# Kernel optimization log

Measured on AMD Instinct MI355X. Metric: run time of the kernel, lower is better.

The kernel has to match this reference:

```python
import jax, jax.numpy as jnp
import numpy as np

B, T, D, H = 2, 2048, 1024, 16
DK = D // H

def setup_inputs() -> dict:
    key = jax.random.key(0)
    ks = jax.random.split(key, 12)
    s = 1.0 / np.sqrt(D)
    inp = {
        'Q': jax.random.normal(ks[0], (B, T, D), jnp.float32),
        'K': jax.random.normal(ks[1], (B, T, D), jnp.float32),
        'V': jax.random.normal(ks[2], (B, T, D), jnp.float32),
        'mask': jnp.tril(jnp.ones((T, T), jnp.int32))[None, None],  # causal [1,1,T,T]
        'Wq_w': jax.random.normal(ks[3], (D, D), jnp.float32) * s,
        'Wq_b': jax.random.normal(ks[4], (D,), jnp.float32) * s,
        'Wk_w': jax.random.normal(ks[5], (D, D), jnp.float32) * s,
        'Wk_b': jax.random.normal(ks[6], (D,), jnp.float32) * s,
        'Wv_w': jax.random.normal(ks[7], (D, D), jnp.float32) * s,
        'Wv_b': jax.random.normal(ks[8], (D,), jnp.float32) * s,
        'Wo_w': jax.random.normal(ks[9], (D, D), jnp.float32) * s,
        'Wo_b': jax.random.normal(ks[10], (D,), jnp.float32) * s,
    }
    return inp

def reference(Q, K, V, mask, Wq_w, Wq_b, Wk_w, Wk_b, Wv_w, Wv_b, Wo_w, Wo_b):
    b, tq, c = Q.shape
    tk = K.shape[1]
    q = (Q @ Wq_w + Wq_b).reshape(b, tq, H, DK).transpose(0, 2, 1, 3)  # [B,H,Tq,dk]
    k = (K @ Wk_w + Wk_b).reshape(b, tk, H, DK).transpose(0, 2, 1, 3)
    v = (V @ Wv_w + Wv_b).reshape(b, tk, H, DK).transpose(0, 2, 1, 3)
    scores = jnp.einsum('bhqd,bhkd->bhqk', q, k) / jnp.sqrt(jnp.float32(DK))
    scores = jnp.where(mask == 0, jnp.float32(-1e9), scores)
    attn = jax.nn.softmax(scores, axis=-1)
    out = jnp.einsum('bhqk,bhkd->bhqd', attn, v)
    out = out.transpose(0, 2, 1, 3).reshape(b, tq, c)
    return out @ Wo_w + Wo_b
```

## Files before the change

kernel.cpp:

```cpp
#include <hip/hip_runtime.h>
#include <hip/hip_bf16.h>

#define NB 2
#define NT 2048
#define ND 1024
#define NH 16
#define NDK 64

typedef __attribute__((ext_vector_type(8))) short bf16x8;
typedef __attribute__((ext_vector_type(4))) float f32x4;

static __device__ __forceinline__ short f2bf(float f) {
  union { float f; unsigned u; } c; c.f = f;
  unsigned u = c.u;
  u += 0x7FFF + ((u >> 16) & 1);
  return (short)(u >> 16);
}

static __device__ __forceinline__ unsigned cvt_pk_bf16(float lo, float hi) {
  unsigned r;
  asm("v_cvt_pk_bf16_f32 %0, %1, %2" : "=v"(r) : "v"(lo), "v"(hi));
  return r;
}

static __device__ __forceinline__ void gload16(const void* g, void* l) {
  __builtin_amdgcn_global_load_lds((const __attribute__((address_space(1))) void*)g,
                                   (__attribute__((address_space(3))) void*)l, 16, 0, 0);
}

__global__ void cast3_kernel(const float* __restrict__ s0, const float* __restrict__ s1,
                             const float* __restrict__ s2,
                             short* __restrict__ t0, short* __restrict__ t1,
                             short* __restrict__ t2) {
  int z = blockIdx.x >> 11;
  int i = (blockIdx.x & 2047) * 256 + threadIdx.x;
  const float* src = z == 0 ? s0 : (z == 1 ? s1 : s2);
  short* dst       = z == 0 ? t0 : (z == 1 ? t1 : t2);
  const float4* s4 = (const float4*)src + (size_t)i * 2;
  float4 a = s4[0], b = s4[1];
  bf16x8 o;
  o[0] = f2bf(a.x); o[1] = f2bf(a.y); o[2] = f2bf(a.z); o[3] = f2bf(a.w);
  o[4] = f2bf(b.x); o[5] = f2bf(b.y); o[6] = f2bf(b.z); o[7] = f2bf(b.w);
  *((bf16x8*)dst + i) = o;
}

__global__ void wtrans_kernel(const float* __restrict__ W0, const float* __restrict__ W1,
                              const float* __restrict__ W2, const float* __restrict__ W3,
                              short* __restrict__ T0, short* __restrict__ T1,
                              short* __restrict__ T2, short* __restrict__ T3) {
  __shared__ float t[32][33];
  int z = blockIdx.z;
  const float* W = z == 0 ? W0 : (z == 1 ? W1 : (z == 2 ? W2 : W3));
  short* Wt      = z == 0 ? T0 : (z == 1 ? T1 : (z == 2 ? T2 : T3));
  int n0 = blockIdx.x * 32, k0 = blockIdx.y * 32;
  int tx = threadIdx.x, ty = threadIdx.y;
  for (int i = ty; i < 32; i += 8) t[i][tx] = W[(size_t)(k0 + i) * ND + n0 + tx];
  __syncthreads();
  for (int i = ty; i < 32; i += 8) Wt[(size_t)(n0 + i) * ND + k0 + tx] = f2bf(t[tx][i]);
}

template <int MODE>
__global__ __launch_bounds__(256, 2) void gemm_bt(
    const short* __restrict__ A0, const short* __restrict__ A1, const short* __restrict__ A2,
    const short* __restrict__ W0, const short* __restrict__ W1, const short* __restrict__ W2,
    const float* __restrict__ b0, const float* __restrict__ b1, const float* __restrict__ b2,
    void* o0, void* o1, void* o2)
{
  constexpr int K = ND;
  __shared__ short As[2][128 * 32];
  __shared__ short Bs[2][128 * 32];
  int z = blockIdx.z;
  const short* A    = z == 0 ? A0 : (z == 1 ? A1 : A2);
  const short* Wt   = z == 0 ? W0 : (z == 1 ? W1 : W2);
  const float* bias = z == 0 ? b0 : (z == 1 ? b1 : b2);
  void* out         = z == 0 ? o0 : (z == 1 ? o1 : o2);
  float scl = (MODE == 0 && z == 0) ? 0.18033688011112042f : 1.0f;

  int m0 = blockIdx.y * 128, n0 = blockIdx.x * 128;
  int tid = threadIdx.x, wid = tid >> 6, lane = tid & 63;
  int wr = wid >> 1, wc = wid & 1;
  int r16 = lane & 15, l4 = lane >> 4;

  auto stage = [&](int buf, int kt) {
    int rbase = wid * 32;
    int row = rbase + (lane >> 2);
    int c8 = (lane & 3) * 8;
    const short* ga = A  + (size_t)(m0 + row) * K + kt * 32 + c8;
    const short* gb = Wt + (size_t)(n0 + row) * K + kt * 32 + c8;
    gload16(ga,          &As[buf][rbase * 32]);
    gload16(ga + 16 * K, &As[buf][(rbase + 16) * 32]);
    gload16(gb,          &Bs[buf][rbase * 32]);
    gload16(gb + 16 * K, &Bs[buf][(rbase + 16) * 32]);
  };

  f32x4 acc[4][4] = {};
  stage(0, 0);
  __syncthreads();

  for (int kt = 0; kt < K / 32; ++kt) {
    int cur = kt & 1;
    if (kt + 1 < K / 32) stage(cur ^ 1, kt + 1);
    bf16x8 af[4], bfv[4];
    int kk = l4 * 8;
#pragma unroll
    for (int mi = 0; mi < 4; mi++)
      af[mi] = *(const bf16x8*)&As[cur][(wr * 64 + mi * 16 + r16) * 32 + kk];
#pragma unroll
    for (int ni = 0; ni < 4; ni++)
      bfv[ni] = *(const bf16x8*)&Bs[cur][(wc * 64 + ni * 16 + r16) * 32 + kk];
#pragma unroll
    for (int mi = 0; mi < 4; mi++)
#pragma unroll
      for (int ni = 0; ni < 4; ni++)
        acc[mi][ni] = __builtin_amdgcn_mfma_f32_16x16x32_bf16(af[mi], bfv[ni], acc[mi][ni], 0, 0, 0);
    __syncthreads();
  }

  int mb = m0 + wr * 64, nb = n0 + wc * 64;
#pragma unroll
  for (int mi = 0; mi < 4; mi++)
#pragma unroll
    for (int ni = 0; ni < 4; ni++) {
      int n = nb + ni * 16 + r16;
      float bv = bias[n];
      if constexpr (MODE == 0) {
        int h = n >> 6, dk = n & 63;
        if (z == 2) {
          int m0_ = mb + mi * 16 + l4 * 4;
          int bI = m0_ >> 11, t0 = m0_ & (NT - 1);
          int bh = bI * NH + h;
          short4 s4;
          s4.x = f2bf(acc[mi][ni][0] + bv);
          s4.y = f2bf(acc[mi][ni][1] + bv);
          s4.z = f2bf(acc[mi][ni][2] + bv);
          s4.w = f2bf(acc[mi][ni][3] + bv);
          *(short4*)&((short*)out)[(size_t)bh * 131072 + (dk >> 4) * 32768 +
                                   (t0 >> 3) * 128 + (dk & 15) * 8 + (t0 & 7)] = s4;
        } else if (z == 1) {
#pragma unroll
          for (int r = 0; r < 4; r++) {
            int m = mb + mi * 16 + l4 * 4 + r;
            int bI = m >> 11, t = m & (NT - 1);
            int bh = bI * NH + h;
            ((short*)out)[(size_t)bh * 131072 + (t >> 4) * 1024 + (dk >> 3) * 128 +
                          (t & 15) * 8 + (dk & 7)] = f2bf(acc[mi][ni][r] + bv);
          }
        } else {
#pragma unroll
          for (int r = 0; r < 4; r++) {
            int m = mb + mi * 16 + l4 * 4 + r;
            int bI = m >> 11, t = m & (NT - 1);
            ((short*)out)[((((size_t)bI * NH + h) * NT + t) << 6) + dk] = f2bf((acc[mi][ni][r] + bv) * scl);
          }
        }
      } else {
#pragma unroll
        for (int r = 0; r < 4; r++) {
          int m = mb + mi * 16 + l4 * 4 + r;
          ((float*)out)[(size_t)m * ND + n] = acc[mi][ni][r] + bv;
        }
      }
    }
}

__global__ __launch_bounds__(256) void attn_kernel(
    const short* __restrict__ q, const short* __restrict__ k, const short* __restrict__ vt,
    short* __restrict__ O)
{
  struct SH {
    union {
      short p2[4][2][16][72];
      struct {
        f32x4 obuf[4][2][4][64];
        float ol[4][32];
      } mg;
    };
  };
  __shared__ SH sh;

  int d = blockIdx.x;
  int xcd = d & 7, jj = d >> 3;
  int bh = xcd * 4 + (jj >> 5);
  int pair = jj & 31;
  int b = bh >> 4, h = bh & 15;
  int tid = threadIdx.x, wid = tid >> 6, lane = tid & 63;
  int r16 = lane & 15, l4 = lane >> 4;
  size_t hb = (size_t)bh * NT * NDK;
  const short* qh = q + hb;
  const short* kh = k + hb;
  const short* vh = vt + hb;

#pragma unroll 1
  for (int half = 0; half < 2; ++half) {
    int qg = half == 0 ? (63 - pair) : pair;
    int qw = qg * 32;

    bf16x8 qa[2][2];
#pragma unroll
    for (int rf = 0; rf < 2; rf++)
#pragma unroll
      for (int kf = 0; kf < 2; kf++)
        qa[rf][kf] = *(const bf16x8*)(qh + (size_t)(qw + rf * 16 + r16) * NDK + kf * 32 + l4 * 8);

    f32x4 of[2][4] = {};
    float l_[2] = { 0.f, 0.f };

    int nt = (qw + 95) >> 6;
    for (int kt = wid; kt < nt; kt += 4) {
      int kv0 = kt * 64;

      f32x4 sf[2][4] = {};
      __builtin_amdgcn_s_setprio(1);
#pragma unroll
      for (int cf = 0; cf < 4; cf++) {
        const short* kb_ = kh + (size_t)((kv0 >> 4) + cf) * 1024 + lane * 8;
        bf16x8 k0 = *(const bf16x8*)kb_;
        bf16x8 k1 = *(const bf16x8*)(kb_ + 512);
        sf[0][cf] = __builtin_amdgcn_mfma_f32_16x16x32_bf16(k0, qa[0][0], sf[0][cf], 0, 0, 0);
        sf[1][cf] = __builtin_amdgcn_mfma_f32_16x16x32_bf16(k0, qa[1][0], sf[1][cf], 0, 0, 0);
        sf[0][cf] = __builtin_amdgcn_mfma_f32_16x16x32_bf16(k1, qa[0][1], sf[0][cf], 0, 0, 0);
        sf[1][cf] = __builtin_amdgcn_mfma_f32_16x16x32_bf16(k1, qa[1][1], sf[1][cf], 0, 0, 0);
      }
      __builtin_amdgcn_s_setprio(0);

      bf16x8 vb[4][2];
#pragma unroll
      for (int df = 0; df < 4; df++)
#pragma unroll
        for (int kf = 0; kf < 2; kf++)
          vb[df][kf] = *(const bf16x8*)(vh + df * 32768 + (kv0 >> 3) * 128 + kf * 512 + lane * 8);

      if (kv0 + 63 > qw) {
#pragma unroll
        for (int rf = 0; rf < 2; rf++)
#pragma unroll
          for (int cf = 0; cf < 4; cf++)
#pragma unroll
            for (int r = 0; r < 4; r++) {
              int kvi = kv0 + cf * 16 + l4 * 4 + r;
              int qi = qw + rf * 16 + r16;
              if (kvi > qi) sf[rf][cf][r] = -1e30f;
            }
      }

#pragma unroll
      for (int rf = 0; rf < 2; rf++) {
        float rs = 0.f;
#pragma unroll
        for (int cf = 0; cf < 4; cf++) {
          float p0 = __builtin_amdgcn_exp2f(sf[rf][cf][0]);
          float p1 = __builtin_amdgcn_exp2f(sf[rf][cf][1]);
          float p2v = __builtin_amdgcn_exp2f(sf[rf][cf][2]);
          float p3 = __builtin_amdgcn_exp2f(sf[rf][cf][3]);
          rs += (p0 + p1) + (p2v + p3);
          unsigned w0 = cvt_pk_bf16(p0, p1);
          unsigned w1 = cvt_pk_bf16(p2v, p3);
          *(int2*)&sh.p2[wid][rf][r16][cf * 16 + l4 * 4] = make_int2((int)w0, (int)w1);
        }
        l_[rf] += rs;
      }

      __builtin_amdgcn_s_setprio(1);
#pragma unroll
      for (int rf = 0; rf < 2; rf++)
#pragma unroll
        for (int kf = 0; kf < 2; kf++) {
          bf16x8 pa = *(const bf16x8*)&sh.p2[wid][rf][r16][kf * 32 + l4 * 8];
#pragma unroll
          for (int df = 0; df < 4; df++)
            of[rf][df] = __builtin_amdgcn_mfma_f32_16x16x32_bf16(vb[df][kf], pa, of[rf][df], 0, 0, 0);
        }
      __builtin_amdgcn_s_setprio(0);
    }

#pragma unroll
    for (int rf = 0; rf < 2; rf++) {
      float t = l_[rf];
      t += __shfl_xor(t, 16);
      t += __shfl_xor(t, 32);
      l_[rf] = t;
    }

    __syncthreads();
#pragma unroll
    for (int rf = 0; rf < 2; rf++) {
      if (l4 == 0) sh.mg.ol[wid][rf * 16 + r16] = l_[rf];
#pragma unroll
      for (int df = 0; df < 4; df++)
        sh.mg.obuf[wid][rf][df][lane] = of[rf][df];
    }
    __syncthreads();

#pragma unroll
    for (int rf = 0; rf < 2; rf++) {
      int row = rf * 16 + r16;
      float lst = sh.mg.ol[0][row] + sh.mg.ol[1][row] + sh.mg.ol[2][row] + sh.mg.ol[3][row];
      float rinv = 1.0f / lst;
      f32x4 o0 = sh.mg.obuf[0][rf][wid][lane];
      f32x4 o1 = sh.mg.obuf[1][rf][wid][lane];
      f32x4 o2 = sh.mg.obuf[2][rf][wid][lane];
      f32x4 o3 = sh.mg.obuf[3][rf][wid][lane];
      float v0 = (o0[0] + o1[0] + o2[0] + o3[0]) * rinv;
      float v1 = (o0[1] + o1[1] + o2[1] + o3[1]) * rinv;
      float v2 = (o0[2] + o1[2] + o2[2] + o3[2]) * rinv;
      float v3 = (o0[3] + o1[3] + o2[3] + o3[3]) * rinv;
      int t = qw + rf * 16 + r16;
      *(int2*)&O[(size_t)(b * NT + t) * ND + h * 64 + wid * 16 + l4 * 4] =
          make_int2((int)cvt_pk_bf16(v0, v1), (int)cvt_pk_bf16(v2, v3));
    }
    __syncthreads();
  }
}

extern "C" void kernel_launch(void* const* d_in, const int* in_sizes, int n_in,
                              void* d_out, int out_size, void* d_ws, size_t ws_size,
                              hipStream_t stream)
{
  const float* Q  = (const float*)d_in[0];
  const float* Ki = (const float*)d_in[1];
  const float* V  = (const float*)d_in[2];
  const float* Wq = (const float*)d_in[4];  const float* bq = (const float*)d_in[5];
  const float* Wk = (const float*)d_in[6];  const float* bk = (const float*)d_in[7];
  const float* Wv = (const float*)d_in[8];  const float* bv = (const float*)d_in[9];
  const float* Wo = (const float*)d_in[10]; const float* bo = (const float*)d_in[11];

  short* ws = (short*)d_ws;
  const size_t M4 = (size_t)4 * 1024 * 1024;
  short* Qb  = ws;
  short* Kb  = ws + M4;
  short* Vb  = ws + 2 * M4;
  short* qp  = ws + 3 * M4;
  short* kp  = ws + 4 * M4;
  short* vtp = ws + 5 * M4;
  short* Wqt = ws + 6 * M4;
  short* Wkt = Wqt + 1024 * 1024;
  short* Wvt = Wkt + 1024 * 1024;
  short* Wot = Wvt + 1024 * 1024;
  short* Obuf = Qb;

  cast3_kernel<<<6144, 256, 0, stream>>>(Q, Ki, V, Qb, Kb, Vb);
  wtrans_kernel<<<dim3(32, 32, 4), dim3(32, 8), 0, stream>>>(Wq, Wk, Wv, Wo,
                                                             Wqt, Wkt, Wvt, Wot);

  gemm_bt<0><<<dim3(8, 32, 3), 256, 0, stream>>>(Qb, Kb, Vb, Wqt, Wkt, Wvt,
                                                 bq, bk, bv, qp, kp, vtp);
  attn_kernel<<<1024, 256, 0, stream>>>(qp, kp, vtp, Obuf);
  gemm_bt<1><<<dim3(8, 32, 1), 256, 0, stream>>>(Obuf, Obuf, Obuf, Wot, Wot, Wot,
                                                 bo, bo, bo, d_out, d_out, d_out);
}
```

Before: 130.3 us.

## Fuse fp32-to-bf16 input cast into projection GEMM and split attention blocks per query tile

Drops the separate cast kernel. The QKV projection GEMM now loads fp32 activations directly, converts them to bf16 in registers and writes them to LDS, which removes one full write and read of the bf16 copies. The attention kernel no longer pairs a long and a short query tile per block. It launches one block per 32-row query tile, so twice as many blocks, and the merge step is done in two passes to halve the LDS buffer. In exchange, the GEMM A-loads become synchronous register loads instead of async global-to-LDS loads, and without the pairing the causal work per block is unbalanced.

```diff
diff --git a/kernel.cpp b/kernel.cpp
--- a/kernel.cpp
+++ b/kernel.cpp
@@ -26,22 +26,6 @@
 static __device__ __forceinline__ void gload16(const void* g, void* l) {
   __builtin_amdgcn_global_load_lds((const __attribute__((address_space(1))) void*)g,
                                    (__attribute__((address_space(3))) void*)l, 16, 0, 0);
-}
-
-__global__ void cast3_kernel(const float* __restrict__ s0, const float* __restrict__ s1,
-                             const float* __restrict__ s2,
-                             short* __restrict__ t0, short* __restrict__ t1,
-                             short* __restrict__ t2) {
-  int z = blockIdx.x >> 11;
-  int i = (blockIdx.x & 2047) * 256 + threadIdx.x;
-  const float* src = z == 0 ? s0 : (z == 1 ? s1 : s2);
-  short* dst       = z == 0 ? t0 : (z == 1 ? t1 : t2);
-  const float4* s4 = (const float4*)src + (size_t)i * 2;
-  float4 a = s4[0], b = s4[1];
-  bf16x8 o;
-  o[0] = f2bf(a.x); o[1] = f2bf(a.y); o[2] = f2bf(a.z); o[3] = f2bf(a.w);
-  o[4] = f2bf(b.x); o[5] = f2bf(b.y); o[6] = f2bf(b.z); o[7] = f2bf(b.w);
-  *((bf16x8*)dst + i) = o;
 }
 
 __global__ void wtrans_kernel(const float* __restrict__ W0, const float* __restrict__ W1,
@@ -61,7 +45,7 @@
 
 template <int MODE>
 __global__ __launch_bounds__(256, 2) void gemm_bt(
-    const short* __restrict__ A0, const short* __restrict__ A1, const short* __restrict__ A2,
+    const void* A0v, const void* A1v, const void* A2v,
     const short* __restrict__ W0, const short* __restrict__ W1, const short* __restrict__ W2,
     const float* __restrict__ b0, const float* __restrict__ b1, const float* __restrict__ b2,
     void* o0, void* o1, void* o2)
@@ -70,10 +54,12 @@
   __shared__ short As[2][128 * 32];
   __shared__ short Bs[2][128 * 32];
   int z = blockIdx.z;
-  const short* A    = z == 0 ? A0 : (z == 1 ? A1 : A2);
+  const void* Av    = z == 0 ? A0v : (z == 1 ? A1v : A2v);
   const short* Wt   = z == 0 ? W0 : (z == 1 ? W1 : W2);
   const float* bias = z == 0 ? b0 : (z == 1 ? b1 : b2);
   void* out         = z == 0 ? o0 : (z == 1 ? o1 : o2);
+  const float* Af = (const float*)Av;
+  const short* Ab = (const short*)Av;
   float scl = (MODE == 0 && z == 0) ? 0.18033688011112042f : 1.0f;
 
   int m0 = blockIdx.y * 128, n0 = blockIdx.x * 128;
@@ -85,10 +71,24 @@
     int rbase = wid * 32;
     int row = rbase + (lane >> 2);
     int c8 = (lane & 3) * 8;
-    const short* ga = A  + (size_t)(m0 + row) * K + kt * 32 + c8;
+    if constexpr (MODE == 0) {
+      const float* ga = Af + (size_t)(m0 + row) * K + kt * 32 + c8;
+      float4 a0 = *(const float4*)ga;
+      float4 a1 = *(const float4*)(ga + 4);
+      float4 a2 = *(const float4*)(ga + (size_t)16 * K);
+      float4 a3 = *(const float4*)(ga + (size_t)16 * K + 4);
+      int4 w0 = make_int4((int)cvt_pk_bf16(a0.x, a0.y), (int)cvt_pk_bf16(a0.z, a0.w),
+                          (int)cvt_pk_bf16(a1.x, a1.y), (int)cvt_pk_bf16(a1.z, a1.w));
+      int4 w1 = make_int4((int)cvt_pk_bf16(a2.x, a2.y), (int)cvt_pk_bf16(a2.z, a2.w),
+                          (int)cvt_pk_bf16(a3.x, a3.y), (int)cvt_pk_bf16(a3.z, a3.w));
+      *(int4*)&As[buf][row * 32 + c8] = w0;
+      *(int4*)&As[buf][(row + 16) * 32 + c8] = w1;
+    } else {
+      const short* ga = Ab + (size_t)(m0 + row) * K + kt * 32 + c8;
+      gload16(ga,          &As[buf][rbase * 32]);
+      gload16(ga + 16 * K, &As[buf][(rbase + 16) * 32]);
+    }
     const short* gb = Wt + (size_t)(n0 + row) * K + kt * 32 + c8;
-    gload16(ga,          &As[buf][rbase * 32]);
-    gload16(ga + 16 * K, &As[buf][(rbase + 16) * 32]);
     gload16(gb,          &Bs[buf][rbase * 32]);
     gload16(gb + 16 * K, &Bs[buf][(rbase + 16) * 32]);
   };
@@ -171,7 +171,7 @@
     union {
       short p2[4][2][16][72];
       struct {
-        f32x4 obuf[4][2][4][64];
+        f32x4 obuf[4][2][2][64];
         float ol[4][32];
       } mg;
     };
@@ -180,8 +180,8 @@
 
   int d = blockIdx.x;
   int xcd = d & 7, jj = d >> 3;
-  int bh = xcd * 4 + (jj >> 5);
-  int pair = jj & 31;
+  int bh = xcd * 4 + (jj >> 6);
+  int qg = 63 - (jj & 63);
   int b = bh >> 4, h = bh & 15;
   int tid = threadIdx.x, wid = tid >> 6, lane = tid & 63;
   int r16 = lane & 15, l4 = lane >> 4;
@@ -189,123 +189,122 @@
   const short* qh = q + hb;
   const short* kh = k + hb;
   const short* vh = vt + hb;
-
-#pragma unroll 1
-  for (int half = 0; half < 2; ++half) {
-    int qg = half == 0 ? (63 - pair) : pair;
-    int qw = qg * 32;
-
-    bf16x8 qa[2][2];
+  int qw = qg * 32;
+
+  bf16x8 qa[2][2];
+#pragma unroll
+  for (int rf = 0; rf < 2; rf++)
+#pragma unroll
+    for (int kf = 0; kf < 2; kf++)
+      qa[rf][kf] = *(const bf16x8*)(qh + (size_t)(qw + rf * 16 + r16) * NDK + kf * 32 + l4 * 8);
+
+  f32x4 of[2][4] = {};
+  float l_[2] = { 0.f, 0.f };
+
+  int nt = (qw + 95) >> 6;
+  for (int kt = wid; kt < nt; kt += 4) {
+    int kv0 = kt * 64;
+
+    f32x4 sf[2][4] = {};
+    __builtin_amdgcn_s_setprio(1);
+#pragma unroll
+    for (int cf = 0; cf < 4; cf++) {
+      const short* kb_ = kh + (size_t)((kv0 >> 4) + cf) * 1024 + lane * 8;
+      bf16x8 k0 = *(const bf16x8*)kb_;
+      bf16x8 k1 = *(const bf16x8*)(kb_ + 512);
+      sf[0][cf] = __builtin_amdgcn_mfma_f32_16x16x32_bf16(k0, qa[0][0], sf[0][cf], 0, 0, 0);
+      sf[1][cf] = __builtin_amdgcn_mfma_f32_16x16x32_bf16(k0, qa[1][0], sf[1][cf], 0, 0, 0);
+      sf[0][cf] = __builtin_amdgcn_mfma_f32_16x16x32_bf16(k1, qa[0][1], sf[0][cf], 0, 0, 0);
+      sf[1][cf] = __builtin_amdgcn_mfma_f32_16x16x32_bf16(k1, qa[1][1], sf[1][cf], 0, 0, 0);
+    }
+    __builtin_amdgcn_s_setprio(0);
+
+    bf16x8 vb[4][2];
+#pragma unroll
+    for (int df = 0; df < 4; df++)
+#pragma unroll
+      for (int kf = 0; kf < 2; kf++)
+        vb[df][kf] = *(const bf16x8*)(vh + df * 32768 + (kv0 >> 3) * 128 + kf * 512 + lane * 8);
+
+    if (kv0 + 63 > qw) {
+#pragma unroll
+      for (int rf = 0; rf < 2; rf++)
+#pragma unroll
+        for (int cf = 0; cf < 4; cf++)
+#pragma unroll
+          for (int r = 0; r < 4; r++) {
+            int kvi = kv0 + cf * 16 + l4 * 4 + r;
+            int qi = qw + rf * 16 + r16;
+            if (kvi > qi) sf[rf][cf][r] = -1e30f;
+          }
+    }
+
+#pragma unroll
+    for (int rf = 0; rf < 2; rf++) {
+      float rs = 0.f;
+#pragma unroll
+      for (int cf = 0; cf < 4; cf++) {
+        float p0 = __builtin_amdgcn_exp2f(sf[rf][cf][0]);
+        float p1 = __builtin_amdgcn_exp2f(sf[rf][cf][1]);
+        float p2v = __builtin_amdgcn_exp2f(sf[rf][cf][2]);
+        float p3 = __builtin_amdgcn_exp2f(sf[rf][cf][3]);
+        rs += (p0 + p1) + (p2v + p3);
+        unsigned w0 = cvt_pk_bf16(p0, p1);
+        unsigned w1 = cvt_pk_bf16(p2v, p3);
+        *(int2*)&sh.p2[wid][rf][r16][cf * 16 + l4 * 4] = make_int2((int)w0, (int)w1);
+      }
+      l_[rf] += rs;
+    }
+
+    __builtin_amdgcn_s_setprio(1);
 #pragma unroll
     for (int rf = 0; rf < 2; rf++)
 #pragma unroll
-      for (int kf = 0; kf < 2; kf++)
-        qa[rf][kf] = *(const bf16x8*)(qh + (size_t)(qw + rf * 16 + r16) * NDK + kf * 32 + l4 * 8);
-
-    f32x4 of[2][4] = {};
-    float l_[2] = { 0.f, 0.f };
-
-    int nt = (qw + 95) >> 6;
-    for (int kt = wid; kt < nt; kt += 4) {
-      int kv0 = kt * 64;
-
-      f32x4 sf[2][4] = {};
-      __builtin_amdgcn_s_setprio(1);
-#pragma unroll
-      for (int cf = 0; cf < 4; cf++) {
-        const short* kb_ = kh + (size_t)((kv0 >> 4) + cf) * 1024 + lane * 8;
-        bf16x8 k0 = *(const bf16x8*)kb_;
-        bf16x8 k1 = *(const bf16x8*)(kb_ + 512);
-        sf[0][cf] = __builtin_amdgcn_mfma_f32_16x16x32_bf16(k0, qa[0][0], sf[0][cf], 0, 0, 0);
-        sf[1][cf] = __builtin_amdgcn_mfma_f32_16x16x32_bf16(k0, qa[1][0], sf[1][cf], 0, 0, 0);
-        sf[0][cf] = __builtin_amdgcn_mfma_f32_16x16x32_bf16(k1, qa[0][1], sf[0][cf], 0, 0, 0);
-        sf[1][cf] = __builtin_amdgcn_mfma_f32_16x16x32_bf16(k1, qa[1][1], sf[1][cf], 0, 0, 0);
+      for (int kf = 0; kf < 2; kf++) {
+        bf16x8 pa = *(const bf16x8*)&sh.p2[wid][rf][r16][kf * 32 + l4 * 8];
+#pragma unroll
+        for (int df = 0; df < 4; df++)
+          of[rf][df] = __builtin_amdgcn_mfma_f32_16x16x32_bf16(vb[df][kf], pa, of[rf][df], 0, 0, 0);
       }
-      __builtin_amdgcn_s_setprio(0);
-
-      bf16x8 vb[4][2];
-#pragma unroll
-      for (int df = 0; df < 4; df++)
-#pragma unroll
-        for (int kf = 0; kf < 2; kf++)
-          vb[df][kf] = *(const bf16x8*)(vh + df * 32768 + (kv0 >> 3) * 128 + kf * 512 + lane * 8);
-
-      if (kv0 + 63 > qw) {
-#pragma unroll
-        for (int rf = 0; rf < 2; rf++)
-#pragma unroll
-          for (int cf = 0; cf < 4; cf++)
-#pragma unroll
-            for (int r = 0; r < 4; r++) {
-              int kvi = kv0 + cf * 16 + l4 * 4 + r;
-              int qi = qw + rf * 16 + r16;
-              if (kvi > qi) sf[rf][cf][r] = -1e30f;
-            }
-      }
-
-#pragma unroll
-      for (int rf = 0; rf < 2; rf++) {
-        float rs = 0.f;
-#pragma unroll
-        for (int cf = 0; cf < 4; cf++) {
-          float p0 = __builtin_amdgcn_exp2f(sf[rf][cf][0]);
-          float p1 = __builtin_amdgcn_exp2f(sf[rf][cf][1]);
-          float p2v = __builtin_amdgcn_exp2f(sf[rf][cf][2]);
-          float p3 = __builtin_amdgcn_exp2f(sf[rf][cf][3]);
-          rs += (p0 + p1) + (p2v + p3);
-          unsigned w0 = cvt_pk_bf16(p0, p1);
-          unsigned w1 = cvt_pk_bf16(p2v, p3);
-          *(int2*)&sh.p2[wid][rf][r16][cf * 16 + l4 * 4] = make_int2((int)w0, (int)w1);
-        }
-        l_[rf] += rs;
-      }
-
-      __builtin_amdgcn_s_setprio(1);
-#pragma unroll
-      for (int rf = 0; rf < 2; rf++)
-#pragma unroll
-        for (int kf = 0; kf < 2; kf++) {
-          bf16x8 pa = *(const bf16x8*)&sh.p2[wid][rf][r16][kf * 32 + l4 * 8];
-#pragma unroll
-          for (int df = 0; df < 4; df++)
-            of[rf][df] = __builtin_amdgcn_mfma_f32_16x16x32_bf16(vb[df][kf], pa, of[rf][df], 0, 0, 0);
-        }
-      __builtin_amdgcn_s_setprio(0);
-    }
-
-#pragma unroll
-    for (int rf = 0; rf < 2; rf++) {
-      float t = l_[rf];
-      t += __shfl_xor(t, 16);
-      t += __shfl_xor(t, 32);
-      l_[rf] = t;
-    }
-
+    __builtin_amdgcn_s_setprio(0);
+  }
+
+#pragma unroll
+  for (int rf = 0; rf < 2; rf++) {
+    float t = l_[rf];
+    t += __shfl_xor(t, 16);
+    t += __shfl_xor(t, 32);
+    l_[rf] = t;
+  }
+
+  __syncthreads();
+  if (l4 == 0) {
+    sh.mg.ol[wid][r16] = l_[0];
+    sh.mg.ol[wid][16 + r16] = l_[1];
+  }
+#pragma unroll
+  for (int pass = 0; pass < 2; ++pass) {
+#pragma unroll
+    for (int rf = 0; rf < 2; rf++)
+#pragma unroll
+      for (int dfp = 0; dfp < 2; dfp++)
+        sh.mg.obuf[wid][rf][dfp][lane] = of[rf][2 * pass + dfp];
     __syncthreads();
-#pragma unroll
-    for (int rf = 0; rf < 2; rf++) {
-      if (l4 == 0) sh.mg.ol[wid][rf * 16 + r16] = l_[rf];
-#pragma unroll
-      for (int df = 0; df < 4; df++)
-        sh.mg.obuf[wid][rf][df][lane] = of[rf][df];
-    }
-    __syncthreads();
-
-#pragma unroll
-    for (int rf = 0; rf < 2; rf++) {
-      int row = rf * 16 + r16;
+    {
+      int mrf = wid >> 1, mdfp = wid & 1, mdf = 2 * pass + mdfp;
+      int row = mrf * 16 + r16;
       float lst = sh.mg.ol[0][row] + sh.mg.ol[1][row] + sh.mg.ol[2][row] + sh.mg.ol[3][row];
       float rinv = 1.0f / lst;
-      f32x4 o0 = sh.mg.obuf[0][rf][wid][lane];
-      f32x4 o1 = sh.mg.obuf[1][rf][wid][lane];
-      f32x4 o2 = sh.mg.obuf[2][rf][wid][lane];
-      f32x4 o3 = sh.mg.obuf[3][rf][wid][lane];
+      f32x4 o0 = sh.mg.obuf[0][mrf][mdfp][lane];
+      f32x4 o1 = sh.mg.obuf[1][mrf][mdfp][lane];
+      f32x4 o2 = sh.mg.obuf[2][mrf][mdfp][lane];
+      f32x4 o3 = sh.mg.obuf[3][mrf][mdfp][lane];
       float v0 = (o0[0] + o1[0] + o2[0] + o3[0]) * rinv;
       float v1 = (o0[1] + o1[1] + o2[1] + o3[1]) * rinv;
       float v2 = (o0[2] + o1[2] + o2[2] + o3[2]) * rinv;
       float v3 = (o0[3] + o1[3] + o2[3] + o3[3]) * rinv;
-      int t = qw + rf * 16 + r16;
-      *(int2*)&O[(size_t)(b * NT + t) * ND + h * 64 + wid * 16 + l4 * 4] =
+      int t = qw + mrf * 16 + r16;
+      *(int2*)&O[(size_t)(b * NT + t) * ND + h * 64 + mdf * 16 + l4 * 4] =
           make_int2((int)cvt_pk_bf16(v0, v1), (int)cvt_pk_bf16(v2, v3));
     }
     __syncthreads();
@@ -326,9 +325,7 @@
 
   short* ws = (short*)d_ws;
   const size_t M4 = (size_t)4 * 1024 * 1024;
-  short* Qb  = ws;
-  short* Kb  = ws + M4;
-  short* Vb  = ws + 2 * M4;
+  short* Obuf = ws;
   short* qp  = ws + 3 * M4;
   short* kp  = ws + 4 * M4;
   short* vtp = ws + 5 * M4;
@@ -336,15 +333,13 @@
   short* Wkt = Wqt + 1024 * 1024;
   short* Wvt = Wkt + 1024 * 1024;
   short* Wot = Wvt + 1024 * 1024;
-  short* Obuf = Qb;
-
-  cast3_kernel<<<6144, 256, 0, stream>>>(Q, Ki, V, Qb, Kb, Vb);
+
   wtrans_kernel<<<dim3(32, 32, 4), dim3(32, 8), 0, stream>>>(Wq, Wk, Wv, Wo,
                                                              Wqt, Wkt, Wvt, Wot);
 
-  gemm_bt<0><<<dim3(8, 32, 3), 256, 0, stream>>>(Qb, Kb, Vb, Wqt, Wkt, Wvt,
+  gemm_bt<0><<<dim3(8, 32, 3), 256, 0, stream>>>(Q, Ki, V, Wqt, Wkt, Wvt,
                                                  bq, bk, bv, qp, kp, vtp);
-  attn_kernel<<<1024, 256, 0, stream>>>(qp, kp, vtp, Obuf);
+  attn_kernel<<<2048, 256, 0, stream>>>(qp, kp, vtp, Obuf);
   gemm_bt<1><<<dim3(8, 32, 1), 256, 0, stream>>>(Obuf, Obuf, Obuf, Wot, Wot, Wot,
                                                  bo, bo, bo, d_out, d_out, d_out);
 }
```

New measurement: 144.3 us. 10.7% more time.

## Launch one attention block per query group and halve merge LDS buffer

Applied to the files above, without the earlier changes.

Removes the paired causal query-group loop so each block handles a single 32-row query group, doubling the grid to 2048 blocks, ordered heaviest-first within each head. The cross-wave merge buffer is halved and the merge runs in two passes, cutting LDS use to allow more resident blocks. This aims at better occupancy and load spreading, at the cost of losing the explicit causal load pairing and adding an extra barrier in the merge.

```diff
diff --git a/kernel.cpp b/kernel.cpp
--- a/kernel.cpp
+++ b/kernel.cpp
@@ -171,7 +171,7 @@
     union {
       short p2[4][2][16][72];
       struct {
-        f32x4 obuf[4][2][4][64];
+        f32x4 obuf[4][2][2][64];
         float ol[4][32];
       } mg;
     };
@@ -180,8 +180,8 @@
 
   int d = blockIdx.x;
   int xcd = d & 7, jj = d >> 3;
-  int bh = xcd * 4 + (jj >> 5);
-  int pair = jj & 31;
+  int bh = xcd * 4 + (jj >> 6);
+  int qg = 63 - (jj & 63);
   int b = bh >> 4, h = bh & 15;
   int tid = threadIdx.x, wid = tid >> 6, lane = tid & 63;
   int r16 = lane & 15, l4 = lane >> 4;
@@ -189,123 +189,122 @@
   const short* qh = q + hb;
   const short* kh = k + hb;
   const short* vh = vt + hb;
-
-#pragma unroll 1
-  for (int half = 0; half < 2; ++half) {
-    int qg = half == 0 ? (63 - pair) : pair;
-    int qw = qg * 32;
-
-    bf16x8 qa[2][2];
+  int qw = qg * 32;
+
+  bf16x8 qa[2][2];
+#pragma unroll
+  for (int rf = 0; rf < 2; rf++)
+#pragma unroll
+    for (int kf = 0; kf < 2; kf++)
+      qa[rf][kf] = *(const bf16x8*)(qh + (size_t)(qw + rf * 16 + r16) * NDK + kf * 32 + l4 * 8);
+
+  f32x4 of[2][4] = {};
+  float l_[2] = { 0.f, 0.f };
+
+  int nt = (qw + 95) >> 6;
+  for (int kt = wid; kt < nt; kt += 4) {
+    int kv0 = kt * 64;
+
+    f32x4 sf[2][4] = {};
+    __builtin_amdgcn_s_setprio(1);
+#pragma unroll
+    for (int cf = 0; cf < 4; cf++) {
+      const short* kb_ = kh + (size_t)((kv0 >> 4) + cf) * 1024 + lane * 8;
+      bf16x8 k0 = *(const bf16x8*)kb_;
+      bf16x8 k1 = *(const bf16x8*)(kb_ + 512);
+      sf[0][cf] = __builtin_amdgcn_mfma_f32_16x16x32_bf16(k0, qa[0][0], sf[0][cf], 0, 0, 0);
+      sf[1][cf] = __builtin_amdgcn_mfma_f32_16x16x32_bf16(k0, qa[1][0], sf[1][cf], 0, 0, 0);
+      sf[0][cf] = __builtin_amdgcn_mfma_f32_16x16x32_bf16(k1, qa[0][1], sf[0][cf], 0, 0, 0);
+      sf[1][cf] = __builtin_amdgcn_mfma_f32_16x16x32_bf16(k1, qa[1][1], sf[1][cf], 0, 0, 0);
+    }
+    __builtin_amdgcn_s_setprio(0);
+
+    bf16x8 vb[4][2];
+#pragma unroll
+    for (int df = 0; df < 4; df++)
+#pragma unroll
+      for (int kf = 0; kf < 2; kf++)
+        vb[df][kf] = *(const bf16x8*)(vh + df * 32768 + (kv0 >> 3) * 128 + kf * 512 + lane * 8);
+
+    if (kv0 + 63 > qw) {
+#pragma unroll
+      for (int rf = 0; rf < 2; rf++)
+#pragma unroll
+        for (int cf = 0; cf < 4; cf++)
+#pragma unroll
+          for (int r = 0; r < 4; r++) {
+            int kvi = kv0 + cf * 16 + l4 * 4 + r;
+            int qi = qw + rf * 16 + r16;
+            if (kvi > qi) sf[rf][cf][r] = -1e30f;
+          }
+    }
+
+#pragma unroll
+    for (int rf = 0; rf < 2; rf++) {
+      float rs = 0.f;
+#pragma unroll
+      for (int cf = 0; cf < 4; cf++) {
+        float p0 = __builtin_amdgcn_exp2f(sf[rf][cf][0]);
+        float p1 = __builtin_amdgcn_exp2f(sf[rf][cf][1]);
+        float p2v = __builtin_amdgcn_exp2f(sf[rf][cf][2]);
+        float p3 = __builtin_amdgcn_exp2f(sf[rf][cf][3]);
+        rs += (p0 + p1) + (p2v + p3);
+        unsigned w0 = cvt_pk_bf16(p0, p1);
+        unsigned w1 = cvt_pk_bf16(p2v, p3);
+        *(int2*)&sh.p2[wid][rf][r16][cf * 16 + l4 * 4] = make_int2((int)w0, (int)w1);
+      }
+      l_[rf] += rs;
+    }
+
+    __builtin_amdgcn_s_setprio(1);
 #pragma unroll
     for (int rf = 0; rf < 2; rf++)
 #pragma unroll
-      for (int kf = 0; kf < 2; kf++)
-        qa[rf][kf] = *(const bf16x8*)(qh + (size_t)(qw + rf * 16 + r16) * NDK + kf * 32 + l4 * 8);
-
-    f32x4 of[2][4] = {};
-    float l_[2] = { 0.f, 0.f };
-
-    int nt = (qw + 95) >> 6;
-    for (int kt = wid; kt < nt; kt += 4) {
-      int kv0 = kt * 64;
-
-      f32x4 sf[2][4] = {};
-      __builtin_amdgcn_s_setprio(1);
-#pragma unroll
-      for (int cf = 0; cf < 4; cf++) {
-        const short* kb_ = kh + (size_t)((kv0 >> 4) + cf) * 1024 + lane * 8;
-        bf16x8 k0 = *(const bf16x8*)kb_;
-        bf16x8 k1 = *(const bf16x8*)(kb_ + 512);
-        sf[0][cf] = __builtin_amdgcn_mfma_f32_16x16x32_bf16(k0, qa[0][0], sf[0][cf], 0, 0, 0);
-        sf[1][cf] = __builtin_amdgcn_mfma_f32_16x16x32_bf16(k0, qa[1][0], sf[1][cf], 0, 0, 0);
-        sf[0][cf] = __builtin_amdgcn_mfma_f32_16x16x32_bf16(k1, qa[0][1], sf[0][cf], 0, 0, 0);
-        sf[1][cf] = __builtin_amdgcn_mfma_f32_16x16x32_bf16(k1, qa[1][1], sf[1][cf], 0, 0, 0);
+      for (int kf = 0; kf < 2; kf++) {
+        bf16x8 pa = *(const bf16x8*)&sh.p2[wid][rf][r16][kf * 32 + l4 * 8];
+#pragma unroll
+        for (int df = 0; df < 4; df++)
+          of[rf][df] = __builtin_amdgcn_mfma_f32_16x16x32_bf16(vb[df][kf], pa, of[rf][df], 0, 0, 0);
       }
-      __builtin_amdgcn_s_setprio(0);
-
-      bf16x8 vb[4][2];
-#pragma unroll
-      for (int df = 0; df < 4; df++)
-#pragma unroll
-        for (int kf = 0; kf < 2; kf++)
-          vb[df][kf] = *(const bf16x8*)(vh + df * 32768 + (kv0 >> 3) * 128 + kf * 512 + lane * 8);
-
-      if (kv0 + 63 > qw) {
-#pragma unroll
-        for (int rf = 0; rf < 2; rf++)
-#pragma unroll
-          for (int cf = 0; cf < 4; cf++)
-#pragma unroll
-            for (int r = 0; r < 4; r++) {
-              int kvi = kv0 + cf * 16 + l4 * 4 + r;
-              int qi = qw + rf * 16 + r16;
-              if (kvi > qi) sf[rf][cf][r] = -1e30f;
-            }
-      }
-
-#pragma unroll
-      for (int rf = 0; rf < 2; rf++) {
-        float rs = 0.f;
-#pragma unroll
-        for (int cf = 0; cf < 4; cf++) {
-          float p0 = __builtin_amdgcn_exp2f(sf[rf][cf][0]);
-          float p1 = __builtin_amdgcn_exp2f(sf[rf][cf][1]);
-          float p2v = __builtin_amdgcn_exp2f(sf[rf][cf][2]);
-          float p3 = __builtin_amdgcn_exp2f(sf[rf][cf][3]);
-          rs += (p0 + p1) + (p2v + p3);
-          unsigned w0 = cvt_pk_bf16(p0, p1);
-          unsigned w1 = cvt_pk_bf16(p2v, p3);
-          *(int2*)&sh.p2[wid][rf][r16][cf * 16 + l4 * 4] = make_int2((int)w0, (int)w1);
-        }
-        l_[rf] += rs;
-      }
-
-      __builtin_amdgcn_s_setprio(1);
-#pragma unroll
-      for (int rf = 0; rf < 2; rf++)
-#pragma unroll
-        for (int kf = 0; kf < 2; kf++) {
-          bf16x8 pa = *(const bf16x8*)&sh.p2[wid][rf][r16][kf * 32 + l4 * 8];
-#pragma unroll
-          for (int df = 0; df < 4; df++)
-            of[rf][df] = __builtin_amdgcn_mfma_f32_16x16x32_bf16(vb[df][kf], pa, of[rf][df], 0, 0, 0);
-        }
-      __builtin_amdgcn_s_setprio(0);
-    }
-
-#pragma unroll
-    for (int rf = 0; rf < 2; rf++) {
-      float t = l_[rf];
-      t += __shfl_xor(t, 16);
-      t += __shfl_xor(t, 32);
-      l_[rf] = t;
-    }
-
+    __builtin_amdgcn_s_setprio(0);
+  }
+
+#pragma unroll
+  for (int rf = 0; rf < 2; rf++) {
+    float t = l_[rf];
+    t += __shfl_xor(t, 16);
+    t += __shfl_xor(t, 32);
+    l_[rf] = t;
+  }
+
+  __syncthreads();
+  if (l4 == 0) {
+    sh.mg.ol[wid][r16] = l_[0];
+    sh.mg.ol[wid][16 + r16] = l_[1];
+  }
+#pragma unroll
+  for (int pass = 0; pass < 2; ++pass) {
+#pragma unroll
+    for (int rf = 0; rf < 2; rf++)
+#pragma unroll
+      for (int dfp = 0; dfp < 2; dfp++)
+        sh.mg.obuf[wid][rf][dfp][lane] = of[rf][2 * pass + dfp];
     __syncthreads();
-#pragma unroll
-    for (int rf = 0; rf < 2; rf++) {
-      if (l4 == 0) sh.mg.ol[wid][rf * 16 + r16] = l_[rf];
-#pragma unroll
-      for (int df = 0; df < 4; df++)
-        sh.mg.obuf[wid][rf][df][lane] = of[rf][df];
-    }
-    __syncthreads();
-
-#pragma unroll
-    for (int rf = 0; rf < 2; rf++) {
-      int row = rf * 16 + r16;
+    {
+      int mrf = wid >> 1, mdfp = wid & 1, mdf = 2 * pass + mdfp;
+      int row = mrf * 16 + r16;
       float lst = sh.mg.ol[0][row] + sh.mg.ol[1][row] + sh.mg.ol[2][row] + sh.mg.ol[3][row];
       float rinv = 1.0f / lst;
-      f32x4 o0 = sh.mg.obuf[0][rf][wid][lane];
-      f32x4 o1 = sh.mg.obuf[1][rf][wid][lane];
-      f32x4 o2 = sh.mg.obuf[2][rf][wid][lane];
-      f32x4 o3 = sh.mg.obuf[3][rf][wid][lane];
+      f32x4 o0 = sh.mg.obuf[0][mrf][mdfp][lane];
+      f32x4 o1 = sh.mg.obuf[1][mrf][mdfp][lane];
+      f32x4 o2 = sh.mg.obuf[2][mrf][mdfp][lane];
+      f32x4 o3 = sh.mg.obuf[3][mrf][mdfp][lane];
       float v0 = (o0[0] + o1[0] + o2[0] + o3[0]) * rinv;
       float v1 = (o0[1] + o1[1] + o2[1] + o3[1]) * rinv;
       float v2 = (o0[2] + o1[2] + o2[2] + o3[2]) * rinv;
       float v3 = (o0[3] + o1[3] + o2[3] + o3[3]) * rinv;
-      int t = qw + rf * 16 + r16;
-      *(int2*)&O[(size_t)(b * NT + t) * ND + h * 64 + wid * 16 + l4 * 4] =
+      int t = qw + mrf * 16 + r16;
+      *(int2*)&O[(size_t)(b * NT + t) * ND + h * 64 + mdf * 16 + l4 * 4] =
           make_int2((int)cvt_pk_bf16(v0, v1), (int)cvt_pk_bf16(v2, v3));
     }
     __syncthreads();
@@ -344,7 +343,7 @@
 
   gemm_bt<0><<<dim3(8, 32, 3), 256, 0, stream>>>(Qb, Kb, Vb, Wqt, Wkt, Wvt,
                                                  bq, bk, bv, qp, kp, vtp);
-  attn_kernel<<<1024, 256, 0, stream>>>(qp, kp, vtp, Obuf);
+  attn_kernel<<<2048, 256, 0, stream>>>(qp, kp, vtp, Obuf);
   gemm_bt<1><<<dim3(8, 32, 1), 256, 0, stream>>>(Obuf, Obuf, Obuf, Wot, Wot, Wot,
                                                  bo, bo, bo, d_out, d_out, d_out);
 }
```

After: 132.1 us. Within noise of the previous version (+1.3%).
